# Performance work log

Measured on AMD Instinct MI355X. Metric: run time of the kernel, lower is better.

## Reference

```python
import jax, jax.numpy as jnp
import numpy as np

N_NODES = 50000
N_EDGES = 800000
IN_DIM = 128
OUT_DIM = 64
HEADS = 8
HEAD_DIM = OUT_DIM // HEADS
NEG_SLOPE = 0.2


def setup_inputs() -> dict:
    key = jax.random.key(0)
    k1, k2, k3, k4, k5 = jax.random.split(key, 5)
    x = jax.random.normal(k1, (N_NODES, IN_DIM), dtype=jnp.float32)
    edge_indices = jax.random.randint(k2, (2, N_EDGES), 0, N_NODES, dtype=jnp.int64)
    # Linear(input_dim, output_dim, bias=False): weight is [out, in]
    W = jax.random.normal(k3, (OUT_DIM, IN_DIM), dtype=jnp.float32) * (1.0 / np.sqrt(IN_DIM))
    src_attn = jax.random.normal(k4, (HEADS, HEAD_DIM), dtype=jnp.float32) * (1.0 / np.sqrt(HEAD_DIM))
    dst_attn = jax.random.normal(k5, (HEADS, HEAD_DIM), dtype=jnp.float32) * (1.0 / np.sqrt(HEAD_DIM))
    return {"x": x, "edge_indices": edge_indices, "W": W, "src_attn": src_attn, "dst_attn": dst_attn}


def reference(x, edge_indices, W, src_attn, dst_attn):
    # Eval mode: all dropouts are identity.
    N = x.shape[0]
    # add self loops
    loops = jnp.arange(N, dtype=edge_indices.dtype)
    ei = jnp.concatenate([edge_indices, jnp.stack([loops, loops])], axis=1)  # [2, E+N]
    row, col = ei[0], ei[1]

    h = (x @ W.T).reshape(N, HEADS, HEAD_DIM)  # [N, H, D]
    s = jnp.einsum("nhd,hd->nh", h, src_attn)  # [N, H]
    d = jnp.einsum("nhd,hd->nh", h, dst_attn)  # [N, H]

    e = jax.nn.leaky_relu(s[row] + d[col], negative_slope=NEG_SLOPE)  # [E', H]

    # segment softmax over rows (torch.sparse.softmax with dim=1 normalizes per row)
    m = jax.ops.segment_max(e, row, num_segments=N)          # [N, H]
    ex = jnp.exp(e - m[row])                                 # [E', H]
    denom = jax.ops.segment_sum(ex, row, num_segments=N)    # [N, H]
    w = ex / denom[row]                                      # [E', H]

    # sparse.mm per head: out[row] += w * h[col]
    msg = w[:, :, None] * h[col]                             # [E', H, D]
    out = jax.ops.segment_sum(msg, row, num_segments=N)      # [N, H, D]
    return out.reshape(N, HEADS * HEAD_DIM)
```

## Files before the change

kernel.cpp:

```cpp
#include <hip/hip_runtime.h>

#define NN 50000
#define IN_DIM 128
#define OUT_DIM 64
#define HEADS 8
#define NEG_SLOPE 0.2f
#define LOG2E 1.44269504088896340736f

#define GEMM_NB ((NN + 63) / 64)
#define NBUCK 196
#define CAP 6144
#define SPLIT 2

typedef __bf16 bf16x8 __attribute__((ext_vector_type(8)));
typedef float f32x4 __attribute__((ext_vector_type(4)));

static __device__ __forceinline__ unsigned short f2bf(float f) {
    __bf16 b = (__bf16)f;
    return __builtin_bit_cast(unsigned short, b);
}
static __device__ __forceinline__ float bf2f(unsigned short u) {
    return __uint_as_float(((unsigned)u) << 16);
}

static __device__ __forceinline__ int detect_i64(const int* __restrict__ ei,
                                                 int lane) {
    unsigned long long b = __ballot(ei[2 * lane + 1] != 0);
    return (b == 0ull) ? 1 : 0;
}

__global__ __launch_bounds__(256) void k_fused0(
        const float* __restrict__ x, const float* __restrict__ W,
        const float* __restrict__ sa, const float* __restrict__ da,
        const int* __restrict__ ei,
        unsigned short* __restrict__ hb, float* __restrict__ s,
        float* __restrict__ d, int* __restrict__ bucketCount,
        unsigned* __restrict__ tmp, int E) {
    __shared__ int hist[NBUCK];
    __shared__ int lpre[NBUCK];
    __shared__ int gbase[NBUCK];
    __shared__ int pref[256];
    __shared__ unsigned lrec[2048];
    __shared__ int tot_s;
    const int tid  = threadIdx.x;
    const int lane = tid & 63;

    if (blockIdx.x >= GEMM_NB) {
        const int bx = blockIdx.x - GEMM_NB;
        if (tid < NBUCK) hist[tid] = 0;
        const int f = detect_i64(ei, lane);
        __syncthreads();

        const int base = bx * 2048 + tid * 8;
        int rw[8], cl[8];
        const bool fullvec = (base + 8 <= E) && ((E & 3) == 0);
        if (f) {
            if (fullvec) {
                const int4* p = (const int4*)(ei + 2 * base);
                const int4* q = (const int4*)(ei + 2 * E + 2 * base);
                #pragma unroll
                for (int g = 0; g < 4; ++g) {
                    int4 a = p[g]; int4 b = q[g];
                    rw[2 * g] = a.x; rw[2 * g + 1] = a.z;
                    cl[2 * g] = b.x; cl[2 * g + 1] = b.z;
                }
            } else {
                #pragma unroll
                for (int k = 0; k < 8; ++k) {
                    int e = base + k;
                    rw[k] = (e < E) ? ei[2 * e] : -1;
                    cl[k] = (e < E) ? ei[2 * E + 2 * e] : 0;
                }
            }
        } else {
            if (fullvec) {
                const int4* p = (const int4*)(ei + base);
                const int4* q = (const int4*)(ei + E + base);
                int4 a0 = p[0], a1 = p[1], b0 = q[0], b1 = q[1];
                rw[0] = a0.x; rw[1] = a0.y; rw[2] = a0.z; rw[3] = a0.w;
                rw[4] = a1.x; rw[5] = a1.y; rw[6] = a1.z; rw[7] = a1.w;
                cl[0] = b0.x; cl[1] = b0.y; cl[2] = b0.z; cl[3] = b0.w;
                cl[4] = b1.x; cl[5] = b1.y; cl[6] = b1.z; cl[7] = b1.w;
            } else {
                #pragma unroll
                for (int k = 0; k < 8; ++k) {
                    int e = base + k;
                    rw[k] = (e < E) ? ei[e] : -1;
                    cl[k] = (e < E) ? ei[E + e] : 0;
                }
            }
        }

        #pragma unroll
        for (int k = 0; k < 8; ++k)
            if (rw[k] >= 0) atomicAdd(&hist[rw[k] >> 8], 1);
        __syncthreads();

        int myCnt = (tid < NBUCK) ? hist[tid] : 0;
        pref[tid] = myCnt;
        __syncthreads();
        for (int off = 1; off < 256; off <<= 1) {
            int u = (tid >= off) ? pref[tid - off] : 0;
            __syncthreads();
            pref[tid] += u;
            __syncthreads();
        }
        if (tid < NBUCK) {
            int ex = pref[tid] - myCnt;
            lpre[tid]  = ex;
            gbase[tid] = tid * CAP + ((myCnt > 0) ? atomicAdd(&bucketCount[tid], myCnt) : 0);
            hist[tid]  = ex;
        }
        if (tid == 255) tot_s = pref[255];
        __syncthreads();

        #pragma unroll
        for (int k = 0; k < 8; ++k) {
            if (rw[k] >= 0) {
                int bk = rw[k] >> 8;
                int lp = atomicAdd(&hist[bk], 1);
                lrec[lp] = ((unsigned)rw[k] << 16) | (unsigned)cl[k];
            }
        }
        __syncthreads();

        const int tot = tot_s;
        for (int j = tid; j < tot; j += 256) {
            unsigned v = lrec[j];
            int row = (int)(v >> 16);
            int bk  = row >> 8;
            int pos = gbase[bk] + (j - lpre[bk]);
            if (pos < (bk + 1) * CAP)
                tmp[pos] = ((unsigned)(row & 255) << 24) | (v & 0xFFFFu);
        }
        return;
    }

    const int wave = tid >> 6;
    const int c    = lane & 15;
    const int kg   = lane >> 4;
    const int n0   = blockIdx.x * 64 + wave * 16;

    bf16x8 bf[4][4];
    #pragma unroll
    for (int kt = 0; kt < 4; ++kt) {
        #pragma unroll
        for (int ot = 0; ot < 4; ++ot) {
            const float* wp = &W[(ot * 16 + c) * 128 + kt * 32 + kg * 8];
            f32x4 w0 = *(const f32x4*)wp;
            f32x4 w1 = *(const f32x4*)(wp + 4);
            bf16x8 b;
            #pragma unroll
            for (int j = 0; j < 4; ++j) { b[j] = (__bf16)w0[j]; b[4 + j] = (__bf16)w1[j]; }
            bf[kt][ot] = b;
        }
    }

    int nr = n0 + c; if (nr > NN - 1) nr = NN - 1;
    const float* xp = &x[(long)nr * 128 + kg * 8];

    f32x4 acc[4] = {};
    #pragma unroll
    for (int kt = 0; kt < 4; ++kt) {
        f32x4 x0 = *(const f32x4*)(xp + kt * 32);
        f32x4 x1 = *(const f32x4*)(xp + kt * 32 + 4);
        bf16x8 a;
        #pragma unroll
        for (int j = 0; j < 4; ++j) { a[j] = (__bf16)x0[j]; a[4 + j] = (__bf16)x1[j]; }
        #pragma unroll
        for (int ot = 0; ot < 4; ++ot)
            acc[ot] = __builtin_amdgcn_mfma_f32_16x16x32_bf16(a, bf[kt][ot], acc[ot], 0, 0, 0);
    }

    float sav[4], dav[4];
    #pragma unroll
    for (int ot = 0; ot < 4; ++ot) {
        sav[ot] = sa[ot * 16 + c] * LOG2E;
        dav[ot] = da[ot * 16 + c] * LOG2E;
    }

    const int nodebase = n0 + kg * 4;
    #pragma unroll
    for (int r = 0; r < 4; ++r) {
        const int n = nodebase + r;
        const bool ok = (n < NN);
        if (ok) {
            #pragma unroll
            for (int ot = 0; ot < 4; ++ot) hb[n * 64 + ot * 16 + c] = f2bf(acc[ot][r]);
        }
        float ps[4], pd[4];
        #pragma unroll
        for (int ot = 0; ot < 4; ++ot) { ps[ot] = acc[ot][r] * sav[ot]; pd[ot] = acc[ot][r] * dav[ot]; }
        #pragma unroll
        for (int m = 1; m < 8; m <<= 1) {
            #pragma unroll
            for (int ot = 0; ot < 4; ++ot) {
                ps[ot] += __shfl_xor(ps[ot], m, 64);
                pd[ot] += __shfl_xor(pd[ot], m, 64);
            }
        }
        if (ok && (c & 7) == 0) {
            const int hbid = c >> 3;
            #pragma unroll
            for (int ot = 0; ot < 4; ++ot) {
                s[n * 8 + 2 * ot + hbid] = ps[ot];
                d[n * 8 + 2 * ot + hbid] = pd[ot];
            }
        }
    }
}

__global__ __launch_bounds__(1024) void k_bgather(
        const unsigned* __restrict__ tmp, const int* __restrict__ bucketCount,
        const unsigned short* __restrict__ hb, const float* __restrict__ sarr,
        const float* __restrict__ d, float* __restrict__ out) {
    __shared__ int bins[256];
    __shared__ int pref[256];
    __shared__ int lcol[CAP];
    const int t    = threadIdx.x;
    const int bkt  = blockIdx.x >> 1;
    const int half = blockIdx.x & 1;
    const int base = bkt * CAP;
    int cnt = bucketCount[bkt]; if (cnt > CAP) cnt = CAP;

    if (t < 256) bins[t] = 0;
    __syncthreads();
    for (int i = t; i < cnt; i += 1024)
        atomicAdd(&bins[tmp[base + i] >> 24], 1);
    __syncthreads();

    if (t < 256) pref[t] = bins[t];
    __syncthreads();
    for (int off = 1; off < 256; off <<= 1) {
        int u = 0;
        if (t < 256 && t >= off) u = pref[t - off];
        __syncthreads();
        if (t < 256) pref[t] += u;
        __syncthreads();
    }
    if (t < 256) bins[t] = pref[t] - bins[t];
    __syncthreads();
    for (int i = t; i < cnt; i += 1024) {
        unsigned v = tmp[base + i];
        int p = atomicAdd(&bins[v >> 24], 1);
        lcol[p] = (int)(v & 0xFFFFFF);
    }
    __syncthreads();

    const int lane = t & 63;
    const int wid  = t >> 6;
    const int o    = lane;
    const int oh   = o >> 3;
    const int eidx = lane >> 3;
    const int h    = lane & 7;

    #pragma unroll
    for (int rr = 0; rr < 256 / (16 * SPLIT); ++rr) {
        const int rl = half * 128 + rr * 16 + wid;
        const int n  = bkt * 256 + rl;
        if (n >= NN) continue;

        const int bgn = (rl == 0) ? 0 : pref[rl - 1];
        const int end = pref[rl];

        const float sn_h = sarr[n * 8 + h];
        float acc  = 0.0f;
        float dsum = 0.0f;

        for (int i = bgn; i < end; i += 8) {
            const int myi  = i + eidx;
            const bool val = (myi < end);
            int c = lcol[val ? myi : (end - 1)];
            float dv = d[c * 8 + h];
            float v = sn_h + dv;
            v = fmaxf(v, NEG_SLOPE * v);
            v = val ? v : -10000.0f;
            float ev = __builtin_amdgcn_exp2f(v);
            dsum += ev;

            #pragma unroll
            for (int k = 0; k < 8; ++k) {
                int   c_k = __builtin_amdgcn_readlane(c, k * 8);
                float e_k = __shfl(ev, k * 8 + oh);
                acc += e_k * bf2f(hb[c_k * 64 + o]);
            }
        }

        dsum += __shfl_xor(dsum, 8, 64);
        dsum += __shfl_xor(dsum, 16, 64);
        dsum += __shfl_xor(dsum, 32, 64);
        float denom = __shfl(dsum, oh);

        const float sn_o = sarr[n * 8 + oh];
        const float dn_o = d[n * 8 + oh];
        float vs = sn_o + dn_o;
        vs = fmaxf(vs, NEG_SLOPE * vs);
        const float es = __builtin_amdgcn_exp2f(vs);
        denom += es;
        acc += es * bf2f(hb[n * 64 + o]);

        out[n * 64 + o] = acc / denom;
    }
}

extern "C" void kernel_launch(void* const* d_in, const int* in_sizes, int n_in,
                              void* d_out, int out_size, void* d_ws, size_t ws_size,
                              hipStream_t stream) {
    const float* x  = (const float*)d_in[0];
    const int*   ei = (const int*)d_in[1];
    const float* W  = (const float*)d_in[2];
    const float* sa = (const float*)d_in[3];
    const float* da = (const float*)d_in[4];
    float* out = (float*)d_out;
    const int E = in_sizes[1] / 2;

    const int NB1 = (E + 2047) / 2048;

    unsigned short* hb = (unsigned short*)d_ws;
    float* s    = (float*)(hb + NN * 64);
    float* dd   = s + NN * 8;
    int*   bucketCount = (int*)(dd + NN * 8);
    unsigned* tmp = (unsigned*)(bucketCount + NBUCK + 4);

    hipMemsetAsync(bucketCount, 0, NBUCK * sizeof(int), stream);
    k_fused0<<<GEMM_NB + NB1, 256, 0, stream>>>(x, W, sa, da, ei,
                                                hb, s, dd, bucketCount, tmp, E);
    k_bgather<<<NBUCK * SPLIT, 1024, 0, stream>>>(tmp, bucketCount, hb, s, dd, out);
}
```

Measured before the change: 74.25 us.

## Merge GEMM, bucketing and gather into one persistent kernel with grid barrier

Replaces the two-kernel pipeline with a single persistent 256-block kernel. Each block runs part of the GEMM, bins its chunk of edges locally and writes per-block bucket counts and offsets, then all blocks meet at an atomic-counter grid barrier. After the barrier each bucket's edges are gathered deterministically from every block's region instead of through a global atomic append. This removes a kernel launch and the global atomics, but adds a spin barrier that needs all 256 blocks of 1024 threads resident at once, plus large LDS use. Gather parallelism also drops from 392 blocks to 196.

```diff
diff --git a/kernel.cpp b/kernel.cpp
--- a/kernel.cpp
+++ b/kernel.cpp
@@ -1,16 +1,14 @@
 #include <hip/hip_runtime.h>
 
 #define NN 50000
-#define IN_DIM 128
-#define OUT_DIM 64
-#define HEADS 8
 #define NEG_SLOPE 0.2f
 #define LOG2E 1.44269504088896340736f
 
-#define GEMM_NB ((NN + 63) / 64)
 #define NBUCK 196
 #define CAP 6144
-#define SPLIT 2
+#define GRID 256
+#define EPB 4096
+#define GEMM_UNITS ((NN + 15) / 16)
 
 typedef __bf16 bf16x8 __attribute__((ext_vector_type(8)));
 typedef float f32x4 __attribute__((ext_vector_type(4)));
@@ -29,44 +27,124 @@
     return (b == 0ull) ? 1 : 0;
 }
 
-__global__ __launch_bounds__(256) void k_fused0(
+static __device__ __forceinline__ void scan256(int* arr, int t) {
+    __syncthreads();
+    for (int off = 1; off < 256; off <<= 1) {
+        int u = 0;
+        if (t < 256 && t >= off) u = arr[t - off];
+        __syncthreads();
+        if (t < 256) arr[t] += u;
+        __syncthreads();
+    }
+}
+
+__global__ __launch_bounds__(1024, 4) void k_mega(
         const float* __restrict__ x, const float* __restrict__ W,
         const float* __restrict__ sa, const float* __restrict__ da,
         const int* __restrict__ ei,
         unsigned short* __restrict__ hb, float* __restrict__ s,
-        float* __restrict__ d, int* __restrict__ bucketCount,
-        unsigned* __restrict__ tmp, int E) {
-    __shared__ int hist[NBUCK];
-    __shared__ int lpre[NBUCK];
-    __shared__ int gbase[NBUCK];
-    __shared__ int pref[256];
-    __shared__ unsigned lrec[2048];
-    __shared__ int tot_s;
-    const int tid  = threadIdx.x;
-    const int lane = tid & 63;
-
-    if (blockIdx.x >= GEMM_NB) {
-        const int bx = blockIdx.x - GEMM_NB;
-        if (tid < NBUCK) hist[tid] = 0;
+        float* __restrict__ d, int* __restrict__ S, int* __restrict__ LP,
+        unsigned* __restrict__ tmp, int* __restrict__ ctr,
+        float* __restrict__ out, int E, int NB1) {
+    __shared__ unsigned u_raw[CAP];
+    __shared__ unsigned u_lcol[CAP];
+    __shared__ int aux1[256];
+    __shared__ int aux2[256];
+    __shared__ int aux3[256];
+
+    const int t    = threadIdx.x;
+    const int lane = t & 63;
+    const int wid  = t >> 6;
+    const int b    = blockIdx.x;
+
+    const int gw = b * 16 + wid;
+    if (gw < GEMM_UNITS) {
+        const int c  = lane & 15;
+        const int kg = lane >> 4;
+        const int n0 = gw * 16;
+
+        bf16x8 bfr[4][4];
+        #pragma unroll
+        for (int kt = 0; kt < 4; ++kt) {
+            #pragma unroll
+            for (int ot = 0; ot < 4; ++ot) {
+                const float* wp = &W[(ot * 16 + c) * 128 + kt * 32 + kg * 8];
+                f32x4 w0 = *(const f32x4*)wp;
+                f32x4 w1 = *(const f32x4*)(wp + 4);
+                bf16x8 bb;
+                #pragma unroll
+                for (int j = 0; j < 4; ++j) { bb[j] = (__bf16)w0[j]; bb[4 + j] = (__bf16)w1[j]; }
+                bfr[kt][ot] = bb;
+            }
+        }
+
+        const float* xp = &x[(long)(n0 + c) * 128 + kg * 8];
+        f32x4 acc[4] = {};
+        #pragma unroll
+        for (int kt = 0; kt < 4; ++kt) {
+            f32x4 x0 = *(const f32x4*)(xp + kt * 32);
+            f32x4 x1 = *(const f32x4*)(xp + kt * 32 + 4);
+            bf16x8 a;
+            #pragma unroll
+            for (int j = 0; j < 4; ++j) { a[j] = (__bf16)x0[j]; a[4 + j] = (__bf16)x1[j]; }
+            #pragma unroll
+            for (int ot = 0; ot < 4; ++ot)
+                acc[ot] = __builtin_amdgcn_mfma_f32_16x16x32_bf16(a, bfr[kt][ot], acc[ot], 0, 0, 0);
+        }
+
+        float sav[4], dav[4];
+        #pragma unroll
+        for (int ot = 0; ot < 4; ++ot) {
+            sav[ot] = sa[ot * 16 + c] * LOG2E;
+            dav[ot] = da[ot * 16 + c] * LOG2E;
+        }
+
+        const int nodebase = n0 + kg * 4;
+        #pragma unroll
+        for (int r = 0; r < 4; ++r) {
+            const int n = nodebase + r;
+            #pragma unroll
+            for (int ot = 0; ot < 4; ++ot) hb[n * 64 + ot * 16 + c] = f2bf(acc[ot][r]);
+            float ps[4], pd[4];
+            #pragma unroll
+            for (int ot = 0; ot < 4; ++ot) { ps[ot] = acc[ot][r] * sav[ot]; pd[ot] = acc[ot][r] * dav[ot]; }
+            #pragma unroll
+            for (int m = 1; m < 8; m <<= 1) {
+                #pragma unroll
+                for (int ot = 0; ot < 4; ++ot) {
+                    ps[ot] += __shfl_xor(ps[ot], m, 64);
+                    pd[ot] += __shfl_xor(pd[ot], m, 64);
+                }
+            }
+            if ((c & 7) == 0) {
+                const int hbid = c >> 3;
+                #pragma unroll
+                for (int ot = 0; ot < 4; ++ot) {
+                    s[n * 8 + 2 * ot + hbid] = ps[ot];
+                    d[n * 8 + 2 * ot + hbid] = pd[ot];
+                }
+            }
+        }
+    }
+
+    if (b < NB1) {
+        if (t < NBUCK) aux1[t] = 0;
         const int f = detect_i64(ei, lane);
         __syncthreads();
 
-        const int base = bx * 2048 + tid * 8;
-        int rw[8], cl[8];
-        const bool fullvec = (base + 8 <= E) && ((E & 3) == 0);
+        const int base = b * EPB + t * 4;
+        int rw[4], cl[4];
+        const bool fullvec = (base + 4 <= E) && ((E & 3) == 0);
         if (f) {
             if (fullvec) {
                 const int4* p = (const int4*)(ei + 2 * base);
                 const int4* q = (const int4*)(ei + 2 * E + 2 * base);
-                #pragma unroll
-                for (int g = 0; g < 4; ++g) {
-                    int4 a = p[g]; int4 b = q[g];
-                    rw[2 * g] = a.x; rw[2 * g + 1] = a.z;
-                    cl[2 * g] = b.x; cl[2 * g + 1] = b.z;
-                }
+                int4 a0 = p[0], a1 = p[1], b0 = q[0], b1 = q[1];
+                rw[0] = a0.x; rw[1] = a0.z; rw[2] = a1.x; rw[3] = a1.z;
+                cl[0] = b0.x; cl[1] = b0.z; cl[2] = b1.x; cl[3] = b1.z;
             } else {
                 #pragma unroll
-                for (int k = 0; k < 8; ++k) {
+                for (int k = 0; k < 4; ++k) {
                     int e = base + k;
                     rw[k] = (e < E) ? ei[2 * e] : -1;
                     cl[k] = (e < E) ? ei[2 * E + 2 * e] : 0;
@@ -74,16 +152,13 @@
             }
         } else {
             if (fullvec) {
-                const int4* p = (const int4*)(ei + base);
-                const int4* q = (const int4*)(ei + E + base);
-                int4 a0 = p[0], a1 = p[1], b0 = q[0], b1 = q[1];
+                int4 a0 = *(const int4*)(ei + base);
+                int4 b0 = *(const int4*)(ei + E + base);
                 rw[0] = a0.x; rw[1] = a0.y; rw[2] = a0.z; rw[3] = a0.w;
-                rw[4] = a1.x; rw[5] = a1.y; rw[6] = a1.z; rw[7] = a1.w;
                 cl[0] = b0.x; cl[1] = b0.y; cl[2] = b0.z; cl[3] = b0.w;
-                cl[4] = b1.x; cl[5] = b1.y; cl[6] = b1.z; cl[7] = b1.w;
             } else {
                 #pragma unroll
-                for (int k = 0; k < 8; ++k) {
+                for (int k = 0; k < 4; ++k) {
                     int e = base + k;
                     rw[k] = (e < E) ? ei[e] : -1;
                     cl[k] = (e < E) ? ei[E + e] : 0;
@@ -92,196 +167,114 @@
         }
 
         #pragma unroll
-        for (int k = 0; k < 8; ++k)
-            if (rw[k] >= 0) atomicAdd(&hist[rw[k] >> 8], 1);
-        __syncthreads();
-
-        int myCnt = (tid < NBUCK) ? hist[tid] : 0;
-        pref[tid] = myCnt;
-        __syncthreads();
-        for (int off = 1; off < 256; off <<= 1) {
-            int u = (tid >= off) ? pref[tid - off] : 0;
-            __syncthreads();
-            pref[tid] += u;
-            __syncthreads();
-        }
-        if (tid < NBUCK) {
-            int ex = pref[tid] - myCnt;
-            lpre[tid]  = ex;
-            gbase[tid] = tid * CAP + ((myCnt > 0) ? atomicAdd(&bucketCount[tid], myCnt) : 0);
-            hist[tid]  = ex;
-        }
-        if (tid == 255) tot_s = pref[255];
-        __syncthreads();
-
-        #pragma unroll
-        for (int k = 0; k < 8; ++k) {
+        for (int k = 0; k < 4; ++k)
+            if (rw[k] >= 0) atomicAdd(&aux1[rw[k] >> 8], 1);
+        __syncthreads();
+
+        const int myCnt = (t < NBUCK) ? aux1[t] : 0;
+        if (t < 256) aux2[t] = myCnt;
+        scan256(aux2, t);
+        if (t < NBUCK) {
+            const int ex = aux2[t] - myCnt;
+            S[t * GRID + b]  = myCnt;
+            LP[t * GRID + b] = ex;
+            aux1[t] = ex;
+        }
+        __syncthreads();
+
+        #pragma unroll
+        for (int k = 0; k < 4; ++k) {
             if (rw[k] >= 0) {
-                int bk = rw[k] >> 8;
-                int lp = atomicAdd(&hist[bk], 1);
-                lrec[lp] = ((unsigned)rw[k] << 16) | (unsigned)cl[k];
-            }
-        }
-        __syncthreads();
-
-        const int tot = tot_s;
-        for (int j = tid; j < tot; j += 256) {
-            unsigned v = lrec[j];
-            int row = (int)(v >> 16);
-            int bk  = row >> 8;
-            int pos = gbase[bk] + (j - lpre[bk]);
-            if (pos < (bk + 1) * CAP)
-                tmp[pos] = ((unsigned)(row & 255) << 24) | (v & 0xFFFFu);
-        }
-        return;
-    }
-
-    const int wave = tid >> 6;
-    const int c    = lane & 15;
-    const int kg   = lane >> 4;
-    const int n0   = blockIdx.x * 64 + wave * 16;
-
-    bf16x8 bf[4][4];
-    #pragma unroll
-    for (int kt = 0; kt < 4; ++kt) {
-        #pragma unroll
-        for (int ot = 0; ot < 4; ++ot) {
-            const float* wp = &W[(ot * 16 + c) * 128 + kt * 32 + kg * 8];
-            f32x4 w0 = *(const f32x4*)wp;
-            f32x4 w1 = *(const f32x4*)(wp + 4);
-            bf16x8 b;
-            #pragma unroll
-            for (int j = 0; j < 4; ++j) { b[j] = (__bf16)w0[j]; b[4 + j] = (__bf16)w1[j]; }
-            bf[kt][ot] = b;
-        }
-    }
-
-    int nr = n0 + c; if (nr > NN - 1) nr = NN - 1;
-    const float* xp = &x[(long)nr * 128 + kg * 8];
-
-    f32x4 acc[4] = {};
-    #pragma unroll
-    for (int kt = 0; kt < 4; ++kt) {
-        f32x4 x0 = *(const f32x4*)(xp + kt * 32);
-        f32x4 x1 = *(const f32x4*)(xp + kt * 32 + 4);
-        bf16x8 a;
-        #pragma unroll
-        for (int j = 0; j < 4; ++j) { a[j] = (__bf16)x0[j]; a[4 + j] = (__bf16)x1[j]; }
-        #pragma unroll
-        for (int ot = 0; ot < 4; ++ot)
-            acc[ot] = __builtin_amdgcn_mfma_f32_16x16x32_bf16(a, bf[kt][ot], acc[ot], 0, 0, 0);
-    }
-
-    float sav[4], dav[4];
-    #pragma unroll
-    for (int ot = 0; ot < 4; ++ot) {
-        sav[ot] = sa[ot * 16 + c] * LOG2E;
-        dav[ot] = da[ot * 16 + c] * LOG2E;
-    }
-
-    const int nodebase = n0 + kg * 4;
-    #pragma unroll
-    for (int r = 0; r < 4; ++r) {
-        const int n = nodebase + r;
-        const bool ok = (n < NN);
-        if (ok) {
-            #pragma unroll
-            for (int ot = 0; ot < 4; ++ot) hb[n * 64 + ot * 16 + c] = f2bf(acc[ot][r]);
-        }
-        float ps[4], pd[4];
-        #pragma unroll
-        for (int ot = 0; ot < 4; ++ot) { ps[ot] = acc[ot][r] * sav[ot]; pd[ot] = acc[ot][r] * dav[ot]; }
-        #pragma unroll
-        for (int m = 1; m < 8; m <<= 1) {
-            #pragma unroll
-            for (int ot = 0; ot < 4; ++ot) {
-                ps[ot] += __shfl_xor(ps[ot], m, 64);
-                pd[ot] += __shfl_xor(pd[ot], m, 64);
-            }
-        }
-        if (ok && (c & 7) == 0) {
-            const int hbid = c >> 3;
-            #pragma unroll
-            for (int ot = 0; ot < 4; ++ot) {
-                s[n * 8 + 2 * ot + hbid] = ps[ot];
-                d[n * 8 + 2 * ot + hbid] = pd[ot];
-            }
-        }
-    }
-}
-
-__global__ __launch_bounds__(1024) void k_bgather(
-        const unsigned* __restrict__ tmp, const int* __restrict__ bucketCount,
-        const unsigned short* __restrict__ hb, const float* __restrict__ sarr,
-        const float* __restrict__ d, float* __restrict__ out) {
-    __shared__ int bins[256];
-    __shared__ int pref[256];
-    __shared__ int lcol[CAP];
-    const int t    = threadIdx.x;
-    const int bkt  = blockIdx.x >> 1;
-    const int half = blockIdx.x & 1;
-    const int base = bkt * CAP;
-    int cnt = bucketCount[bkt]; if (cnt > CAP) cnt = CAP;
-
-    if (t < 256) bins[t] = 0;
+                const int bk = rw[k] >> 8;
+                const int lp = atomicAdd(&aux1[bk], 1);
+                u_raw[lp] = ((unsigned)(rw[k] & 255) << 24) | (unsigned)cl[k];
+            }
+        }
+        __syncthreads();
+        const int tot = aux2[255];
+        for (int j = t; j < tot; j += 1024)
+            tmp[b * EPB + j] = u_raw[j];
+    }
+
+    __syncthreads();
+    if (t == 0) {
+        __builtin_amdgcn_fence(__ATOMIC_RELEASE, "agent");
+        atomicAdd(ctr, 1);
+        while (atomicAdd(ctr, 0) < GRID) __builtin_amdgcn_s_sleep(2);
+        __builtin_amdgcn_fence(__ATOMIC_ACQUIRE, "agent");
+    }
+    __syncthreads();
+
+    if (b >= NBUCK) return;
+    const int bkt = b;
+
+    const int scnt = (t < NB1) ? S[bkt * GRID + t] : 0;
+    if (t < 256) aux2[t] = scnt;
+    scan256(aux2, t);
+    if (t < 256) aux3[t] = aux2[t] - scnt;
+    __syncthreads();
+
+    for (int bx = wid; bx < NB1; bx += 16) {
+        const int dst0   = aux3[bx];
+        const int cnt_bx = aux2[bx] - dst0;
+        const int src0   = bx * EPB + LP[bkt * GRID + bx];
+        for (int j = lane; j < cnt_bx; j += 64) {
+            const int dp = dst0 + j;
+            if (dp < CAP) u_raw[dp] = tmp[src0 + j];
+        }
+    }
+    __syncthreads();
+    int cnt = aux2[255]; if (cnt > CAP) cnt = CAP;
+
+    if (t < 256) aux1[t] = 0;
     __syncthreads();
     for (int i = t; i < cnt; i += 1024)
-        atomicAdd(&bins[tmp[base + i] >> 24], 1);
-    __syncthreads();
-
-    if (t < 256) pref[t] = bins[t];
-    __syncthreads();
-    for (int off = 1; off < 256; off <<= 1) {
-        int u = 0;
-        if (t < 256 && t >= off) u = pref[t - off];
-        __syncthreads();
-        if (t < 256) pref[t] += u;
-        __syncthreads();
-    }
-    if (t < 256) bins[t] = pref[t] - bins[t];
+        atomicAdd(&aux1[u_raw[i] >> 24], 1);
+    __syncthreads();
+    const int rb = (t < 256) ? aux1[t] : 0;
+    if (t < 256) aux2[t] = rb;
+    scan256(aux2, t);
+    if (t < 256) aux1[t] = aux2[t] - rb;
     __syncthreads();
     for (int i = t; i < cnt; i += 1024) {
-        unsigned v = tmp[base + i];
-        int p = atomicAdd(&bins[v >> 24], 1);
-        lcol[p] = (int)(v & 0xFFFFFF);
-    }
-    __syncthreads();
-
-    const int lane = t & 63;
-    const int wid  = t >> 6;
+        const unsigned v = u_raw[i];
+        const int p = atomicAdd(&aux1[(int)(v >> 24)], 1);
+        u_lcol[p] = v & 0xFFFFFFu;
+    }
+    __syncthreads();
+
     const int o    = lane;
     const int oh   = o >> 3;
     const int eidx = lane >> 3;
     const int h    = lane & 7;
 
-    #pragma unroll
-    for (int rr = 0; rr < 256 / (16 * SPLIT); ++rr) {
-        const int rl = half * 128 + rr * 16 + wid;
+    for (int j = 0; j < 16; ++j) {
+        const int rl = j * 16 + wid;
         const int n  = bkt * 256 + rl;
         if (n >= NN) continue;
 
-        const int bgn = (rl == 0) ? 0 : pref[rl - 1];
-        const int end = pref[rl];
-
-        const float sn_h = sarr[n * 8 + h];
+        const int bgn = rl ? aux2[rl - 1] : 0;
+        const int end = aux2[rl];
+
+        const float sn_h = s[n * 8 + h];
         float acc  = 0.0f;
         float dsum = 0.0f;
 
         for (int i = bgn; i < end; i += 8) {
             const int myi  = i + eidx;
             const bool val = (myi < end);
-            int c = lcol[val ? myi : (end - 1)];
-            float dv = d[c * 8 + h];
+            const int cc = (int)u_lcol[val ? myi : (end - 1)];
+            float dv = d[cc * 8 + h];
             float v = sn_h + dv;
             v = fmaxf(v, NEG_SLOPE * v);
             v = val ? v : -10000.0f;
-            float ev = __builtin_amdgcn_exp2f(v);
+            const float ev = __builtin_amdgcn_exp2f(v);
             dsum += ev;
 
             #pragma unroll
             for (int k = 0; k < 8; ++k) {
-                int   c_k = __builtin_amdgcn_readlane(c, k * 8);
-                float e_k = __shfl(ev, k * 8 + oh);
+                const int   c_k = __builtin_amdgcn_readlane(cc, k * 8);
+                const float e_k = __shfl(ev, k * 8 + oh);
                 acc += e_k * bf2f(hb[c_k * 64 + o]);
             }
         }
@@ -291,7 +284,7 @@
         dsum += __shfl_xor(dsum, 32, 64);
         float denom = __shfl(dsum, oh);
 
-        const float sn_o = sarr[n * 8 + oh];
+        const float sn_o = s[n * 8 + oh];
         const float dn_o = d[n * 8 + oh];
         float vs = sn_o + dn_o;
         vs = fmaxf(vs, NEG_SLOPE * vs);
@@ -314,16 +307,18 @@
     float* out = (float*)d_out;
     const int E = in_sizes[1] / 2;
 
-    const int NB1 = (E + 2047) / 2048;
+    int NB1 = (E + EPB - 1) / EPB;
+    if (NB1 > GRID) NB1 = GRID;
 
     unsigned short* hb = (unsigned short*)d_ws;
-    float* s    = (float*)(hb + NN * 64);
-    float* dd   = s + NN * 8;
-    int*   bucketCount = (int*)(dd + NN * 8);
-    unsigned* tmp = (unsigned*)(bucketCount + NBUCK + 4);
-
-    hipMemsetAsync(bucketCount, 0, NBUCK * sizeof(int), stream);
-    k_fused0<<<GEMM_NB + NB1, 256, 0, stream>>>(x, W, sa, da, ei,
-                                                hb, s, dd, bucketCount, tmp, E);
-    k_bgather<<<NBUCK * SPLIT, 1024, 0, stream>>>(tmp, bucketCount, hb, s, dd, out);
-}
+    float* s  = (float*)(hb + NN * 64);
+    float* dd = s + NN * 8;
+    int* S    = (int*)(dd + NN * 8);
+    int* LP   = S + NBUCK * GRID;
+    unsigned* tmp = (unsigned*)(LP + NBUCK * GRID);
+    int* ctr  = (int*)(tmp + (size_t)GRID * EPB);
+
+    hipMemsetAsync(ctr, 0, sizeof(int), stream);
+    k_mega<<<GRID, 1024, 0, stream>>>(x, W, sa, da, ei, hb, s, dd,
+                                      S, LP, tmp, ctr, out, E, NB1);
+}
```

Result: slower. 105.2 us (+41.7%).

## Replace global bucket atomics with per-block count tables and gather-side compaction

Applied to the files above, without the earlier changes.

The edge-bucketing stage no longer reserves space in global buckets with atomics. Each block now writes its locally sorted edge records contiguously, plus per-bucket count and offset tables. The gather kernel prefix-sums those tables, pulls its bucket's segments from every source block into shared memory, and sub-sorts only its own half of the rows. This drops the global atomics and the scattered writes, and lets the memset go. In exchange each gather block does many small strided reads across up to 256 segments, and both halves redundantly load the whole bucket. Edges are silently dropped if NB1 is capped at 256 (when E exceeds 256*4096) or if a bucket exceeds CAPF or a half exceeds CAPH.

```diff
diff --git a/kernel.cpp b/kernel.cpp
--- a/kernel.cpp
+++ b/kernel.cpp
@@ -1,16 +1,14 @@
 #include <hip/hip_runtime.h>
 
 #define NN 50000
-#define IN_DIM 128
-#define OUT_DIM 64
-#define HEADS 8
 #define NEG_SLOPE 0.2f
 #define LOG2E 1.44269504088896340736f
 
 #define GEMM_NB ((NN + 63) / 64)
 #define NBUCK 196
-#define CAP 6144
-#define SPLIT 2
+#define EPB 4096
+#define CAPF 4608
+#define CAPH 2816
 
 typedef __bf16 bf16x8 __attribute__((ext_vector_type(8)));
 typedef float f32x4 __attribute__((ext_vector_type(4)));
@@ -34,39 +32,36 @@
         const float* __restrict__ sa, const float* __restrict__ da,
         const int* __restrict__ ei,
         unsigned short* __restrict__ hb, float* __restrict__ s,
-        float* __restrict__ d, int* __restrict__ bucketCount,
-        unsigned* __restrict__ tmp, int E) {
-    __shared__ int hist[NBUCK];
-    __shared__ int lpre[NBUCK];
-    __shared__ int gbase[NBUCK];
+        float* __restrict__ d, int* __restrict__ S, int* __restrict__ LP,
+        unsigned* __restrict__ tmp, int E, int NB1) {
+    __shared__ int hist[256];
     __shared__ int pref[256];
-    __shared__ unsigned lrec[2048];
-    __shared__ int tot_s;
+    __shared__ unsigned lrec[EPB];
     const int tid  = threadIdx.x;
     const int lane = tid & 63;
 
     if (blockIdx.x >= GEMM_NB) {
         const int bx = blockIdx.x - GEMM_NB;
-        if (tid < NBUCK) hist[tid] = 0;
+        hist[tid] = 0;
         const int f = detect_i64(ei, lane);
         __syncthreads();
 
-        const int base = bx * 2048 + tid * 8;
-        int rw[8], cl[8];
-        const bool fullvec = (base + 8 <= E) && ((E & 3) == 0);
+        const int base = bx * EPB + tid * 16;
+        int rw[16], cl[16];
+        const bool fullvec = (base + 16 <= E) && ((E & 3) == 0);
         if (f) {
             if (fullvec) {
                 const int4* p = (const int4*)(ei + 2 * base);
                 const int4* q = (const int4*)(ei + 2 * E + 2 * base);
                 #pragma unroll
-                for (int g = 0; g < 4; ++g) {
+                for (int g = 0; g < 8; ++g) {
                     int4 a = p[g]; int4 b = q[g];
                     rw[2 * g] = a.x; rw[2 * g + 1] = a.z;
                     cl[2 * g] = b.x; cl[2 * g + 1] = b.z;
                 }
             } else {
                 #pragma unroll
-                for (int k = 0; k < 8; ++k) {
+                for (int k = 0; k < 16; ++k) {
                     int e = base + k;
                     rw[k] = (e < E) ? ei[2 * e] : -1;
                     cl[k] = (e < E) ? ei[2 * E + 2 * e] : 0;
@@ -76,14 +71,17 @@
             if (fullvec) {
                 const int4* p = (const int4*)(ei + base);
                 const int4* q = (const int4*)(ei + E + base);
-                int4 a0 = p[0], a1 = p[1], b0 = q[0], b1 = q[1];
-                rw[0] = a0.x; rw[1] = a0.y; rw[2] = a0.z; rw[3] = a0.w;
-                rw[4] = a1.x; rw[5] = a1.y; rw[6] = a1.z; rw[7] = a1.w;
-                cl[0] = b0.x; cl[1] = b0.y; cl[2] = b0.z; cl[3] = b0.w;
-                cl[4] = b1.x; cl[5] = b1.y; cl[6] = b1.z; cl[7] = b1.w;
+                #pragma unroll
+                for (int g = 0; g < 4; ++g) {
+                    int4 a = p[g]; int4 b = q[g];
+                    rw[4 * g] = a.x; rw[4 * g + 1] = a.y;
+                    rw[4 * g + 2] = a.z; rw[4 * g + 3] = a.w;
+                    cl[4 * g] = b.x; cl[4 * g + 1] = b.y;
+                    cl[4 * g + 2] = b.z; cl[4 * g + 3] = b.w;
+                }
             } else {
                 #pragma unroll
-                for (int k = 0; k < 8; ++k) {
+                for (int k = 0; k < 16; ++k) {
                     int e = base + k;
                     rw[k] = (e < E) ? ei[e] : -1;
                     cl[k] = (e < E) ? ei[E + e] : 0;
@@ -92,11 +90,11 @@
         }
 
         #pragma unroll
-        for (int k = 0; k < 8; ++k)
+        for (int k = 0; k < 16; ++k)
             if (rw[k] >= 0) atomicAdd(&hist[rw[k] >> 8], 1);
         __syncthreads();
 
-        int myCnt = (tid < NBUCK) ? hist[tid] : 0;
+        const int myCnt = hist[tid];
         pref[tid] = myCnt;
         __syncthreads();
         for (int off = 1; off < 256; off <<= 1) {
@@ -106,33 +104,24 @@
             __syncthreads();
         }
         if (tid < NBUCK) {
-            int ex = pref[tid] - myCnt;
-            lpre[tid]  = ex;
-            gbase[tid] = tid * CAP + ((myCnt > 0) ? atomicAdd(&bucketCount[tid], myCnt) : 0);
-            hist[tid]  = ex;
-        }
-        if (tid == 255) tot_s = pref[255];
-        __syncthreads();
-
-        #pragma unroll
-        for (int k = 0; k < 8; ++k) {
+            S[tid * NB1 + bx]  = myCnt;
+            LP[tid * NB1 + bx] = pref[tid] - myCnt;
+        }
+        hist[tid] = pref[tid] - myCnt;
+        __syncthreads();
+
+        #pragma unroll
+        for (int k = 0; k < 16; ++k) {
             if (rw[k] >= 0) {
-                int bk = rw[k] >> 8;
-                int lp = atomicAdd(&hist[bk], 1);
-                lrec[lp] = ((unsigned)rw[k] << 16) | (unsigned)cl[k];
-            }
-        }
-        __syncthreads();
-
-        const int tot = tot_s;
-        for (int j = tid; j < tot; j += 256) {
-            unsigned v = lrec[j];
-            int row = (int)(v >> 16);
-            int bk  = row >> 8;
-            int pos = gbase[bk] + (j - lpre[bk]);
-            if (pos < (bk + 1) * CAP)
-                tmp[pos] = ((unsigned)(row & 255) << 24) | (v & 0xFFFFu);
-        }
+                int lp = atomicAdd(&hist[rw[k] >> 8], 1);
+                lrec[lp] = ((unsigned)(rw[k] & 255) << 24) | (unsigned)cl[k];
+            }
+        }
+        __syncthreads();
+
+        const int tot = pref[255];
+        for (int j = tid; j < tot; j += 256)
+            tmp[bx * EPB + j] = lrec[j];
         return;
     }
 
@@ -211,57 +200,90 @@
 }
 
 __global__ __launch_bounds__(1024) void k_bgather(
-        const unsigned* __restrict__ tmp, const int* __restrict__ bucketCount,
-        const unsigned short* __restrict__ hb, const float* __restrict__ sarr,
-        const float* __restrict__ d, float* __restrict__ out) {
-    __shared__ int bins[256];
-    __shared__ int pref[256];
-    __shared__ int lcol[CAP];
+        const unsigned* __restrict__ tmp, const int* __restrict__ S,
+        const int* __restrict__ LP, const unsigned short* __restrict__ hb,
+        const float* __restrict__ sarr, const float* __restrict__ d,
+        float* __restrict__ out, int NB1) {
+    __shared__ int aux2[256];
+    __shared__ int aux3[256];
+    __shared__ int bins[128];
+    __shared__ int pref2[128];
+    __shared__ unsigned u_raw[CAPF];
+    __shared__ int lcol[CAPH];
+
     const int t    = threadIdx.x;
     const int bkt  = blockIdx.x >> 1;
     const int half = blockIdx.x & 1;
-    const int base = bkt * CAP;
-    int cnt = bucketCount[bkt]; if (cnt > CAP) cnt = CAP;
-
-    if (t < 256) bins[t] = 0;
-    __syncthreads();
-    for (int i = t; i < cnt; i += 1024)
-        atomicAdd(&bins[tmp[base + i] >> 24], 1);
-    __syncthreads();
-
-    if (t < 256) pref[t] = bins[t];
+    const int lane = t & 63;
+    const int wid  = t >> 6;
+
+    if (t < 256) {
+        aux2[t] = (t < NB1) ? S[bkt * NB1 + t] : 0;
+        aux3[t] = (t < NB1) ? LP[bkt * NB1 + t] : 0;
+    }
     __syncthreads();
     for (int off = 1; off < 256; off <<= 1) {
         int u = 0;
-        if (t < 256 && t >= off) u = pref[t - off];
-        __syncthreads();
-        if (t < 256) pref[t] += u;
-        __syncthreads();
-    }
-    if (t < 256) bins[t] = pref[t] - bins[t];
+        if (t < 256 && t >= off) u = aux2[t - off];
+        __syncthreads();
+        if (t < 256) aux2[t] += u;
+        __syncthreads();
+    }
+
+    for (int bx = wid; bx < NB1; bx += 16) {
+        const int dst0 = bx ? aux2[bx - 1] : 0;
+        const int cbx  = aux2[bx] - dst0;
+        const int src0 = bx * EPB + aux3[bx];
+        for (int j = lane; j < cbx; j += 64) {
+            const int dp = dst0 + j;
+            if (dp < CAPF) u_raw[dp] = tmp[src0 + j];
+        }
+    }
+    __syncthreads();
+    int cnt = aux2[255]; if (cnt > CAPF) cnt = CAPF;
+
+    if (t < 128) bins[t] = 0;
     __syncthreads();
     for (int i = t; i < cnt; i += 1024) {
-        unsigned v = tmp[base + i];
-        int p = atomicAdd(&bins[v >> 24], 1);
-        lcol[p] = (int)(v & 0xFFFFFF);
-    }
-    __syncthreads();
-
-    const int lane = t & 63;
-    const int wid  = t >> 6;
+        const int r8 = (int)(u_raw[i] >> 24);
+        if ((r8 >> 7) == half) atomicAdd(&bins[r8 & 127], 1);
+    }
+    __syncthreads();
+    const int bv = (t < 128) ? bins[t] : 0;
+    if (t < 128) pref2[t] = bv;
+    __syncthreads();
+    for (int off = 1; off < 128; off <<= 1) {
+        int u = 0;
+        if (t < 128 && t >= off) u = pref2[t - off];
+        __syncthreads();
+        if (t < 128) pref2[t] += u;
+        __syncthreads();
+    }
+    if (t < 128) bins[t] = pref2[t] - bv;
+    __syncthreads();
+    for (int i = t; i < cnt; i += 1024) {
+        const unsigned v = u_raw[i];
+        const int r8 = (int)(v >> 24);
+        if ((r8 >> 7) == half) {
+            const int p = atomicAdd(&bins[r8 & 127], 1);
+            if (p < CAPH) lcol[p] = (int)(v & 0xFFFFu);
+        }
+    }
+    __syncthreads();
+
     const int o    = lane;
     const int oh   = o >> 3;
     const int eidx = lane >> 3;
     const int h    = lane & 7;
 
     #pragma unroll
-    for (int rr = 0; rr < 256 / (16 * SPLIT); ++rr) {
-        const int rl = half * 128 + rr * 16 + wid;
-        const int n  = bkt * 256 + rl;
+    for (int j = 0; j < 8; ++j) {
+        const int rl = j * 16 + wid;
+        const int n  = bkt * 256 + half * 128 + rl;
         if (n >= NN) continue;
 
-        const int bgn = (rl == 0) ? 0 : pref[rl - 1];
-        const int end = pref[rl];
+        const int bgn = rl ? pref2[rl - 1] : 0;
+        const int end = pref2[rl];
 
         const float sn_h = sarr[n * 8 + h];
         float acc  = 0.0f;
@@ -270,18 +292,18 @@
         for (int i = bgn; i < end; i += 8) {
             const int myi  = i + eidx;
             const bool val = (myi < end);
-            int c = lcol[val ? myi : (end - 1)];
+            const int c = lcol[val ? myi : (end - 1)];
             float dv = d[c * 8 + h];
             float v = sn_h + dv;
             v = fmaxf(v, NEG_SLOPE * v);
             v = val ? v : -10000.0f;
-            float ev = __builtin_amdgcn_exp2f(v);
+            const float ev = __builtin_amdgcn_exp2f(v);
             dsum += ev;
 
             #pragma unroll
             for (int k = 0; k < 8; ++k) {
-                int   c_k = __builtin_amdgcn_readlane(c, k * 8);
-                float e_k = __shfl(ev, k * 8 + oh);
+                const int   c_k = __builtin_amdgcn_readlane(c, k * 8);
+                const float e_k = __shfl(ev, k * 8 + oh);
                 acc += e_k * bf2f(hb[c_k * 64 + o]);
             }
         }
@@ -314,16 +336,17 @@
     float* out = (float*)d_out;
     const int E = in_sizes[1] / 2;
 
-    const int NB1 = (E + 2047) / 2048;
+    int NB1 = (E + EPB - 1) / EPB;
+    if (NB1 > 256) NB1 = 256;
 
     unsigned short* hb = (unsigned short*)d_ws;
-    float* s    = (float*)(hb + NN * 64);
-    float* dd   = s + NN * 8;
-    int*   bucketCount = (int*)(dd + NN * 8);
-    unsigned* tmp = (unsigned*)(bucketCount + NBUCK + 4);
-
-    hipMemsetAsync(bucketCount, 0, NBUCK * sizeof(int), stream);
+    float* s  = (float*)(hb + NN * 64);
+    float* dd = s + NN * 8;
+    int* S    = (int*)(dd + NN * 8);
+    int* LP   = S + NBUCK * 256;
+    unsigned* tmp = (unsigned*)(LP + NBUCK * 256);
+
     k_fused0<<<GEMM_NB + NB1, 256, 0, stream>>>(x, W, sa, da, ei,
-                                                hb, s, dd, bucketCount, tmp, E);
-    k_bgather<<<NBUCK * SPLIT, 1024, 0, stream>>>(tmp, bucketCount, hb, s, dd, out);
-}
+                                                hb, s, dd, S, LP, tmp, E, NB1);
+    k_bgather<<<NBUCK * 2, 1024, 0, stream>>>(tmp, S, LP, hb, s, dd, out, NB1);
+}
```

Result: faster. 71.51 us (-3.7%).
